# Kernel optimization log

Hardware: AMD Instinct MI355X
Metric: run time of the kernel (lower is better)

Reference implementation:

```python
import jax, jax.numpy as jnp
import numpy as np

EPS = 1e-5

def setup_inputs() -> dict:
    key = jax.random.key(0)
    ks = jax.random.split(key, 10)
    B, C, H, W, D = 1, 128, 20, 20, 20
    Cq = C // 8
    s = 0.05
    return {
        "x":   jax.random.normal(ks[0], (B, C, H, W, D), jnp.float32),
        "wq":  jax.random.normal(ks[1], (Cq, C), jnp.float32) * s,
        "bq":  jnp.zeros((Cq,), jnp.float32),
        "wk":  jax.random.normal(ks[2], (Cq, C), jnp.float32) * s,
        "bk":  jnp.zeros((Cq,), jnp.float32),
        "wv":  jax.random.normal(ks[3], (C, C), jnp.float32) * s,
        "bv":  jnp.zeros((C,), jnp.float32),
        "wa":  jax.random.normal(ks[4], (C, C), jnp.float32) * s,
        "ba":  jnp.zeros((C,), jnp.float32),
        "bn_w": jnp.ones((C,), jnp.float32),
        "bn_b": jnp.zeros((C,), jnp.float32),
    }

def reference(x, wq, bq, wk, bk, wv, bv, wa, ba, bn_w, bn_b):
    B, C, H, W, D = x.shape
    N = H * W * D
    xf = x.reshape(B, C, N)                                   # (B,C,N)
    # 1x1 conv projections = per-position channel matmuls
    q = jnp.einsum('oc,bcn->bno', wq, xf) + bq                # (B,N,Cq)
    k = jnp.einsum('oc,bcn->bon', wk, xf) + bk[:, None]       # (B,Cq,N)
    v = jnp.einsum('oc,bcn->bon', wv, xf) + bv[:, None]       # (B,C,N)
    # raw (unscaled) attention, softmax over key positions
    att = jax.nn.softmax(jnp.einsum('bnc,bcm->bnm', q, k), axis=-1)  # (B,N,N)
    # att_value[b,c,i] = sum_j value[b,c,j] * att[b,i,j]
    av = jnp.einsum('bcj,bij->bci', v, att)                   # (B,C,N)
    y = jnp.einsum('oc,bcn->bon', wa, av) + ba[:, None]       # (B,C,N)
    # BatchNorm (training mode): per-channel stats over batch + spatial
    mean = jnp.mean(y, axis=(0, 2), keepdims=True)
    var = jnp.var(y, axis=(0, 2), keepdims=True)
    y = (y - mean) * jax.lax.rsqrt(var + EPS) * bn_w[:, None] + bn_b[:, None]
    out = jax.nn.relu(y) + xf
    return out.reshape(B, C, H, W, D)
```

## Files before the change

### kernel.cpp

```cpp
#include <hip/hip_runtime.h>
#include <math.h>

#define N_POS 8000

typedef __bf16 bf16x8 __attribute__((ext_vector_type(8)));
typedef float  f32x4  __attribute__((ext_vector_type(4)));

#define MFMA(a,b,c) __builtin_amdgcn_mfma_f32_16x16x32_bf16((a),(b),(c),0,0,0)


#define GLOAD_LDS(gp, lp) \
    __builtin_amdgcn_global_load_lds( \
        (const __attribute__((address_space(1))) void*)(gp), \
        (__attribute__((address_space(3))) void*)(lp), 16, 0, 0)

__global__ __launch_bounds__(256) void qkv_kernel(
    const float* __restrict__ x,
    const float* __restrict__ wq, const float* __restrict__ bq,
    const float* __restrict__ wk, const float* __restrict__ bk,
    const float* __restrict__ wv, const float* __restrict__ bv,
    __bf16* __restrict__ q_bf, __bf16* __restrict__ k_bf, __bf16* __restrict__ v_bf)
{
    __shared__ __bf16 x_lds[32 * 136];
    __shared__ __bf16 v_out[128 * 36];

    const int t    = threadIdx.x;
    const int n0   = blockIdx.x * 32;
    const int lane = t & 63;
    const int w    = t >> 6;
    const int l15  = lane & 15;
    const int quad = lane >> 4;

    for (int r = 0; r < 4; ++r) {
        int f = r * 256 + t;
        int ch = f >> 3, n4 = f & 7;
        float4 xv = *reinterpret_cast<const float4*>(&x[ch * N_POS + n0 + n4 * 4]);
        x_lds[(n4 * 4 + 0) * 136 + ch] = (__bf16)xv.x;
        x_lds[(n4 * 4 + 1) * 136 + ch] = (__bf16)xv.y;
        x_lds[(n4 * 4 + 2) * 136 + ch] = (__bf16)xv.z;
        x_lds[(n4 * 4 + 3) * 136 + ch] = (__bf16)xv.w;
    }

    bf16x8 aw[3][4];
    f32x4  acc[3][2];
    const int nmt = (w < 2) ? 3 : 2;
    for (int mi = 0; mi < nmt; ++mi) {
        int mt = w + 4 * mi;
        const float *wrow, *brow;
        if (mt == 0)      { wrow = wq + l15 * 128;               brow = bq; }
        else if (mt == 1) { wrow = wk + l15 * 128;               brow = bk; }
        else              { wrow = wv + ((mt - 2) * 16 + l15) * 128;
                            brow = bv + (mt - 2) * 16; }
        for (int ks = 0; ks < 4; ++ks) {
            float4 f0 = *reinterpret_cast<const float4*>(wrow + ks * 32 + quad * 8);
            float4 f1 = *reinterpret_cast<const float4*>(wrow + ks * 32 + quad * 8 + 4);
            bf16x8 a;
            a[0]=(__bf16)f0.x; a[1]=(__bf16)f0.y; a[2]=(__bf16)f0.z; a[3]=(__bf16)f0.w;
            a[4]=(__bf16)f1.x; a[5]=(__bf16)f1.y; a[6]=(__bf16)f1.z; a[7]=(__bf16)f1.w;
            aw[mi][ks] = a;
        }
        for (int ni = 0; ni < 2; ++ni) {
            acc[mi][ni][0] = brow[quad * 4 + 0]; acc[mi][ni][1] = brow[quad * 4 + 1];
            acc[mi][ni][2] = brow[quad * 4 + 2]; acc[mi][ni][3] = brow[quad * 4 + 3];
        }
    }
    __syncthreads();

    for (int ks = 0; ks < 4; ++ks) {
        bf16x8 b0 = *reinterpret_cast<const bf16x8*>(&x_lds[(0  + l15) * 136 + ks * 32 + quad * 8]);
        bf16x8 b1 = *reinterpret_cast<const bf16x8*>(&x_lds[(16 + l15) * 136 + ks * 32 + quad * 8]);
        for (int mi = 0; mi < nmt; ++mi) {
            acc[mi][0] = MFMA(aw[mi][ks], b0, acc[mi][0]);
            acc[mi][1] = MFMA(aw[mi][ks], b1, acc[mi][1]);
        }
    }

    union S4 { short4 s; __bf16 b[4]; };
    for (int mi = 0; mi < nmt; ++mi) {
        int mt = w + 4 * mi;
        for (int ni = 0; ni < 2; ++ni) {
            S4 u;
            u.b[0]=(__bf16)acc[mi][ni][0]; u.b[1]=(__bf16)acc[mi][ni][1];
            u.b[2]=(__bf16)acc[mi][ni][2]; u.b[3]=(__bf16)acc[mi][ni][3];
            int n = n0 + ni * 16 + l15;
            if (mt == 0) {
                *reinterpret_cast<short4*>(&q_bf[n * 16 + quad * 4]) = u.s;
            } else if (mt == 1) {
                *reinterpret_cast<short4*>(&k_bf[n * 16 + quad * 4]) = u.s;
            } else {
                int ch0 = (mt - 2) * 16 + quad * 4;
                int nl  = ni * 16 + l15;
                v_out[(ch0 + 0) * 36 + nl] = u.b[0];
                v_out[(ch0 + 1) * 36 + nl] = u.b[1];
                v_out[(ch0 + 2) * 36 + nl] = u.b[2];
                v_out[(ch0 + 3) * 36 + nl] = u.b[3];
            }
        }
    }
    __syncthreads();
    for (int r = 0; r < 4; ++r) {
        int f = r * 256 + t;
        int ch = f >> 3, n4 = f & 7;
        int2 d = *reinterpret_cast<const int2*>(&v_out[ch * 36 + n4 * 4]);
        *reinterpret_cast<int2*>(&v_bf[ch * N_POS + n0 + n4 * 4]) = d;
    }
}

__global__ __launch_bounds__(256, 4) void attn_kernel(
    const __bf16* __restrict__ q_bf, const __bf16* __restrict__ k_bf,
    const __bf16* __restrict__ v_bf, float* __restrict__ av_part,
    float* __restrict__ l_part, int nsplit)
{
    __shared__ __bf16 v_buf[2][8192];
    __shared__ __bf16 k_buf[2][1024];
    __shared__ __bf16 p_lds[2048];

    const int t    = threadIdx.x;
    const int qt   = blockIdx.x % 250;
    const int sp   = blockIdx.x / 250;
    const int n0q  = qt * 32;
    const int lane = t & 63;
    const int w    = t >> 6;
    const int l15  = lane & 15;
    const int quad = lane >> 4;

    const int chL   = lane >> 3;
    const int vpart = (lane & 7) ^ chL;
    const int kkey  = lane >> 1;
    const int khalf = lane & 1;

    bf16x8 aq[2];
    for (int ni = 0; ni < 2; ++ni) {
        for (int j = 0; j < 8; ++j) aq[ni][j] = (__bf16)0.0f;
        if (quad < 2)
            aq[ni] = *reinterpret_cast<const bf16x8*>(
                &q_bf[(n0q + ni * 16 + l15) * 16 + quad * 8]);
    }
    bf16x8 ones;
    for (int j = 0; j < 8; ++j) ones[j] = (__bf16)1.0f;

    f32x4 acc[2][2];
    for (int mi = 0; mi < 2; ++mi)
        for (int ni = 0; ni < 2; ++ni)
            for (int r = 0; r < 4; ++r) acc[mi][ni][r] = 0.f;
    f32x4 lacc[2];
    for (int ni = 0; ni < 2; ++ni)
        for (int r = 0; r < 4; ++r) lacc[ni][r] = 0.f;

    const int base = 125 / nsplit, rem = 125 - base * nsplit;
    const int kt0  = sp * base + (sp < rem ? sp : rem);
    const int cnt  = base + (sp < rem ? 1 : 0);

    auto stage = [&](int kt, int buf) {
        const int n0k = kt * 64;
        for (int r = 0; r < 4; ++r) {
            int R = w * 4 + r;
            GLOAD_LDS(v_bf + (8 * R + chL) * N_POS + n0k + vpart * 8,
                      &v_buf[buf][R * 512]);
        }
        for (int h = 0; h < 2; ++h) {
            GLOAD_LDS(k_bf + (size_t)(n0k + h * 32 + kkey) * 16 + khalf * 8,
                      &k_buf[buf][h * 512]);
        }
    };

    stage(kt0, 0);

    const int oS  = w * 2 + (quad >> 1);
    const int sub = (quad & 1) * 4;

    for (int it = 0; it < cnt; ++it) {
        const int kt  = kt0 + it;
        const int cur = it & 1;
        __syncthreads();

        bf16x8 ak;
        for (int j = 0; j < 8; ++j) ak[j] = (__bf16)0.0f;
        if (quad < 2)
            ak = *reinterpret_cast<const bf16x8*>(
                &k_buf[cur][(w * 16 + l15) * 16 + quad * 8]);
        f32x4 s0, s1;
        for (int r = 0; r < 4; ++r) { s0[r] = 0.f; s1[r] = 0.f; }
        s0 = MFMA(ak, aq[0], s0);
        s1 = MFMA(ak, aq[1], s1);
        union SH { short4 sh; __bf16 b[4]; };
        {
            SH u;
            u.b[0] = (__bf16)__expf(s0[0]); u.b[1] = (__bf16)__expf(s0[1]);
            u.b[2] = (__bf16)__expf(s0[2]); u.b[3] = (__bf16)__expf(s0[3]);
            *reinterpret_cast<short4*>(&p_lds[(oS * 32 + l15) * 8 + sub]) = u.sh;
            u.b[0] = (__bf16)__expf(s1[0]); u.b[1] = (__bf16)__expf(s1[1]);
            u.b[2] = (__bf16)__expf(s1[2]); u.b[3] = (__bf16)__expf(s1[3]);
            *reinterpret_cast<short4*>(&p_lds[(oS * 32 + 16 + l15) * 8 + sub]) = u.sh;
        }
        __syncthreads();

        if (it + 1 < cnt) stage(kt + 1, cur ^ 1);

        const int chl = l15 & 7;
        for (int ks = 0; ks < 2; ++ks) {
            int pz = ((ks * 4 + quad) ^ chl);
            bf16x8 a0 = *reinterpret_cast<const bf16x8*>(
                &v_buf[cur][(((2 * w)     * 2 + (l15 >> 3)) * 64 + chl * 8 + pz) * 8]);
            bf16x8 a1 = *reinterpret_cast<const bf16x8*>(
                &v_buf[cur][(((2 * w + 1) * 2 + (l15 >> 3)) * 64 + chl * 8 + pz) * 8]);
            bf16x8 p0 = *reinterpret_cast<const bf16x8*>(
                &p_lds[((ks * 4 + quad) * 32 + 0  + l15) * 8]);
            bf16x8 p1 = *reinterpret_cast<const bf16x8*>(
                &p_lds[((ks * 4 + quad) * 32 + 16 + l15) * 8]);
            acc[0][0] = MFMA(a0, p0, acc[0][0]);
            acc[0][1] = MFMA(a0, p1, acc[0][1]);
            acc[1][0] = MFMA(a1, p0, acc[1][0]);
            acc[1][1] = MFMA(a1, p1, acc[1][1]);
            if (w == 0) {
                lacc[0] = MFMA(ones, p0, lacc[0]);
                lacc[1] = MFMA(ones, p1, lacc[1]);
            }
        }
    }

    float* dst = av_part + (size_t)sp * 1024000;
    for (int mi = 0; mi < 2; ++mi)
        for (int ni = 0; ni < 2; ++ni) {
            int n  = n0q + ni * 16 + l15;
            int ch = (2 * w + mi) * 16 + quad * 4;
            *reinterpret_cast<f32x4*>(&dst[n * 128 + ch]) = acc[mi][ni];
        }
    if (w == 0 && quad == 0) {
        l_part[sp * N_POS + n0q + 0  + l15] = lacc[0][0];
        l_part[sp * N_POS + n0q + 16 + l15] = lacc[1][0];
    }
}

__global__ __launch_bounds__(256) void proj_out_kernel(
    const float* __restrict__ av_part, const float* __restrict__ l_part,
    const float* __restrict__ wa, const float* __restrict__ ba,
    float* __restrict__ y_ws, float* __restrict__ bn_sum, float* __restrict__ bn_sumsq,
    int nsplit)
{
    __shared__ __bf16 b_lds[4096];

    const int t    = threadIdx.x;
    const int n0   = blockIdx.x * 32;
    const int lane = t & 63;
    const int w    = t >> 6;
    const int l15  = lane & 15;
    const int quad = lane >> 4;

    for (int r = 0; r < 2; ++r) {
        int g = r * 256 + t;
        int n = g >> 4, oc = g & 15;
        float l = 0.f;
        for (int s = 0; s < nsplit; ++s) l += l_part[s * N_POS + n0 + n];
        float4 a0 = make_float4(0.f, 0.f, 0.f, 0.f);
        float4 a1 = make_float4(0.f, 0.f, 0.f, 0.f);
        for (int s = 0; s < nsplit; ++s) {
            const float* p = av_part + (size_t)s * 1024000 + (n0 + n) * 128 + oc * 8;
            float4 u = *reinterpret_cast<const float4*>(p);
            float4 v = *reinterpret_cast<const float4*>(p + 4);
            a0.x += u.x; a0.y += u.y; a0.z += u.z; a0.w += u.w;
            a1.x += v.x; a1.y += v.y; a1.z += v.z; a1.w += v.w;
        }
        float inv = 1.f / l;
        union { int4 iv; __bf16 b[8]; } u;
        u.b[0]=(__bf16)(a0.x*inv); u.b[1]=(__bf16)(a0.y*inv);
        u.b[2]=(__bf16)(a0.z*inv); u.b[3]=(__bf16)(a0.w*inv);
        u.b[4]=(__bf16)(a1.x*inv); u.b[5]=(__bf16)(a1.y*inv);
        u.b[6]=(__bf16)(a1.z*inv); u.b[7]=(__bf16)(a1.w*inv);
        int A = (n >> 4) * 16 + oc;
        int slot = (n & 15) ^ (oc & 7);
        *reinterpret_cast<int4*>(&b_lds[(A * 16 + slot) * 8]) = u.iv;
    }

    bf16x8 aw[2][4];
    f32x4  acc[2][2];
    for (int mi = 0; mi < 2; ++mi) {
        int mt = 2 * w + mi;
        const float* wrow = wa + (mt * 16 + l15) * 128;
        for (int ks = 0; ks < 4; ++ks) {
            float4 f0 = *reinterpret_cast<const float4*>(wrow + ks * 32 + quad * 8);
            float4 f1 = *reinterpret_cast<const float4*>(wrow + ks * 32 + quad * 8 + 4);
            bf16x8 a;
            a[0]=(__bf16)f0.x; a[1]=(__bf16)f0.y; a[2]=(__bf16)f0.z; a[3]=(__bf16)f0.w;
            a[4]=(__bf16)f1.x; a[5]=(__bf16)f1.y; a[6]=(__bf16)f1.z; a[7]=(__bf16)f1.w;
            aw[mi][ks] = a;
        }
        for (int ni = 0; ni < 2; ++ni) {
            acc[mi][ni][0] = ba[mt * 16 + quad * 4 + 0];
            acc[mi][ni][1] = ba[mt * 16 + quad * 4 + 1];
            acc[mi][ni][2] = ba[mt * 16 + quad * 4 + 2];
            acc[mi][ni][3] = ba[mt * 16 + quad * 4 + 3];
        }
    }
    __syncthreads();

    for (int ks = 0; ks < 4; ++ks) {
        int oc = ks * 4 + quad;
        int slot = l15 ^ (oc & 7);
        bf16x8 b0 = *reinterpret_cast<const bf16x8*>(&b_lds[((0  + oc) * 16 + slot) * 8]);
        bf16x8 b1 = *reinterpret_cast<const bf16x8*>(&b_lds[((16 + oc) * 16 + slot) * 8]);
        for (int mi = 0; mi < 2; ++mi) {
            acc[mi][0] = MFMA(aw[mi][ks], b0, acc[mi][0]);
            acc[mi][1] = MFMA(aw[mi][ks], b1, acc[mi][1]);
        }
    }

    for (int mi = 0; mi < 2; ++mi) {
        for (int r = 0; r < 4; ++r) {
            int ch = (2 * w + mi) * 16 + quad * 4 + r;
            float v0 = acc[mi][0][r];
            float v1 = acc[mi][1][r];
            y_ws[ch * N_POS + n0 + 0  + l15] = v0;
            y_ws[ch * N_POS + n0 + 16 + l15] = v1;
            float s1 = v0 + v1;
            float s2 = v0 * v0 + v1 * v1;
#pragma unroll
            for (int off = 8; off >= 1; off >>= 1) {
                s1 += __shfl_xor(s1, off, 64);
                s2 += __shfl_xor(s2, off, 64);
            }
            if (l15 == 0) {
                atomicAdd(&bn_sum[ch],   s1);
                atomicAdd(&bn_sumsq[ch], s2);
            }
        }
    }
}

__global__ __launch_bounds__(256) void bn_relu_kernel(
    const float* __restrict__ y_ws, const float* __restrict__ x,
    const float* __restrict__ bn_sum, const float* __restrict__ bn_sumsq,
    const float* __restrict__ bn_w, const float* __restrict__ bn_b,
    float* __restrict__ out)
{
    const int i4 = blockIdx.x * 256 + threadIdx.x;
    const int c  = i4 / 2000;
    const float mean  = bn_sum[c]   * (1.f / 8000.f);
    const float var   = bn_sumsq[c] * (1.f / 8000.f) - mean * mean;
    const float rstd  = rsqrtf(var + 1e-5f);
    const float scale = bn_w[c] * rstd;
    const float shift = bn_b[c] - mean * scale;

    float4 y4 = reinterpret_cast<const float4*>(y_ws)[i4];
    float4 x4 = reinterpret_cast<const float4*>(x)[i4];
    float4 o4;
    o4.x = fmaxf(y4.x * scale + shift, 0.f) + x4.x;
    o4.y = fmaxf(y4.y * scale + shift, 0.f) + x4.y;
    o4.z = fmaxf(y4.z * scale + shift, 0.f) + x4.z;
    o4.w = fmaxf(y4.w * scale + shift, 0.f) + x4.w;
    reinterpret_cast<float4*>(out)[i4] = o4;
}

extern "C" void kernel_launch(void* const* d_in, const int* in_sizes, int n_in,
                              void* d_out, int out_size, void* d_ws, size_t ws_size,
                              hipStream_t stream)
{
    const float* x    = (const float*)d_in[0];
    const float* wq   = (const float*)d_in[1];
    const float* bq   = (const float*)d_in[2];
    const float* wk   = (const float*)d_in[3];
    const float* bk   = (const float*)d_in[4];
    const float* wv   = (const float*)d_in[5];
    const float* bv   = (const float*)d_in[6];
    const float* wa   = (const float*)d_in[7];
    const float* ba   = (const float*)d_in[8];
    const float* bn_w = (const float*)d_in[9];
    const float* bn_b = (const float*)d_in[10];
    float* out = (float*)d_out;

    const int nsplit = (ws_size >= 47937024ull) ? 10 : 5;

    char* base = (char*)d_ws;
    size_t avB = (size_t)nsplit * 4096000;
    float*  av_part = (float*)base;
    __bf16* q_bf    = (__bf16*)(base + avB);
    __bf16* k_bf    = (__bf16*)(base + avB + 256000);
    __bf16* v_bf    = (__bf16*)(base + avB + 512000);
    float*  l_part  = (float*)(base + avB + 2560000);
    float*  bn_sum   = (float*)(base + avB + 2560000 + (size_t)nsplit * 32000);
    float*  bn_sumsq = bn_sum + 128;
    float*  y_ws    = (float*)(base + avB + 2560000 + (size_t)nsplit * 32000 + 1024);

    hipMemsetAsync(bn_sum, 0, 1024, stream);
    qkv_kernel<<<250, 256, 0, stream>>>(x, wq, bq, wk, bk, wv, bv, q_bf, k_bf, v_bf);
    attn_kernel<<<250 * nsplit, 256, 0, stream>>>(q_bf, k_bf, v_bf,
                                                  av_part, l_part, nsplit);
    proj_out_kernel<<<250, 256, 0, stream>>>(av_part, l_part, wa, ba,
                                             y_ws, bn_sum, bn_sumsq, nsplit);
    bn_relu_kernel<<<1000, 256, 0, stream>>>(y_ws, x, bn_sum, bn_sumsq,
                                             bn_w, bn_b, out);
}
```

Baseline: 178.3 us.

## Store split attention partials in bf16 and double grid of qkv and projection kernels

Attention split-K partial outputs are now written as bf16 instead of fp32, halving the partial-buffer traffic between the attention and output-projection kernels. The qkv and output-projection kernels launch twice as many blocks, each doing half the channel tiles or 16 positions, to raise occupancy. The BN stats memset is folded into the qkv kernel, and the split count is fixed at 10 regardless of workspace size. Rounding partials to bf16 before the reduction adds some precision loss, and the fixed layout assumes the workspace is large enough.

```diff
diff --git a/kernel.cpp b/kernel.cpp
--- a/kernel.cpp
+++ b/kernel.cpp
@@ -2,6 +2,7 @@
 #include <math.h>
 
 #define N_POS 8000
+#define NSPLIT 10
 
 typedef __bf16 bf16x8 __attribute__((ext_vector_type(8)));
 typedef float  f32x4  __attribute__((ext_vector_type(4)));
@@ -19,17 +20,22 @@
     const float* __restrict__ wq, const float* __restrict__ bq,
     const float* __restrict__ wk, const float* __restrict__ bk,
     const float* __restrict__ wv, const float* __restrict__ bv,
-    __bf16* __restrict__ q_bf, __bf16* __restrict__ k_bf, __bf16* __restrict__ v_bf)
+    __bf16* __restrict__ q_bf, __bf16* __restrict__ k_bf, __bf16* __restrict__ v_bf,
+    float* __restrict__ bn_stats)
 {
     __shared__ __bf16 x_lds[32 * 136];
-    __shared__ __bf16 v_out[128 * 36];
+    __shared__ __bf16 v_out[80 * 36];
 
     const int t    = threadIdx.x;
-    const int n0   = blockIdx.x * 32;
+    const int nt   = blockIdx.x >> 1;
+    const int h    = blockIdx.x & 1;
+    const int n0   = nt * 32;
     const int lane = t & 63;
     const int w    = t >> 6;
     const int l15  = lane & 15;
     const int quad = lane >> 4;
+
+    if (blockIdx.x == 0) bn_stats[t] = 0.f;
 
     for (int r = 0; r < 4; ++r) {
         int f = r * 256 + t;
@@ -41,11 +47,13 @@
         x_lds[(n4 * 4 + 3) * 136 + ch] = (__bf16)xv.w;
     }
 
-    bf16x8 aw[3][4];
-    f32x4  acc[3][2];
-    const int nmt = (w < 2) ? 3 : 2;
+    const int nmt = (w == 0) ? 2 : 1;
+    int mts[2] = { h * 5 + w, h * 5 + 4 };
+
+    bf16x8 aw[2][4];
+    f32x4  acc[2][2];
     for (int mi = 0; mi < nmt; ++mi) {
-        int mt = w + 4 * mi;
+        int mt = mts[mi];
         const float *wrow, *brow;
         if (mt == 0)      { wrow = wq + l15 * 128;               brow = bq; }
         else if (mt == 1) { wrow = wk + l15 * 128;               brow = bk; }
@@ -77,7 +85,7 @@
 
     union S4 { short4 s; __bf16 b[4]; };
     for (int mi = 0; mi < nmt; ++mi) {
-        int mt = w + 4 * mi;
+        int mt = mts[mi];
         for (int ni = 0; ni < 2; ++ni) {
             S4 u;
             u.b[0]=(__bf16)acc[mi][ni][0]; u.b[1]=(__bf16)acc[mi][ni][1];
@@ -88,27 +96,27 @@
             } else if (mt == 1) {
                 *reinterpret_cast<short4*>(&k_bf[n * 16 + quad * 4]) = u.s;
             } else {
-                int ch0 = (mt - 2) * 16 + quad * 4;
-                int nl  = ni * 16 + l15;
-                v_out[(ch0 + 0) * 36 + nl] = u.b[0];
-                v_out[(ch0 + 1) * 36 + nl] = u.b[1];
-                v_out[(ch0 + 2) * 36 + nl] = u.b[2];
-                v_out[(ch0 + 3) * 36 + nl] = u.b[3];
+                int lv = (mt - 2) * 16 - h * 48 + quad * 4;
+                int nl = ni * 16 + l15;
+                v_out[(lv + 0) * 36 + nl] = u.b[0];
+                v_out[(lv + 1) * 36 + nl] = u.b[1];
+                v_out[(lv + 2) * 36 + nl] = u.b[2];
+                v_out[(lv + 3) * 36 + nl] = u.b[3];
             }
         }
     }
     __syncthreads();
-    for (int r = 0; r < 4; ++r) {
-        int f = r * 256 + t;
-        int ch = f >> 3, n4 = f & 7;
-        int2 d = *reinterpret_cast<const int2*>(&v_out[ch * 36 + n4 * 4]);
-        *reinterpret_cast<int2*>(&v_bf[ch * N_POS + n0 + n4 * 4]) = d;
+    const int nch = h ? 80 : 48;
+    for (int f = t; f < nch * 8; f += 256) {
+        int lc = f >> 3, n4 = f & 7;
+        int2 d = *reinterpret_cast<const int2*>(&v_out[lc * 36 + n4 * 4]);
+        *reinterpret_cast<int2*>(&v_bf[(lc + h * 48) * N_POS + n0 + n4 * 4]) = d;
     }
 }
 
 __global__ __launch_bounds__(256, 4) void attn_kernel(
     const __bf16* __restrict__ q_bf, const __bf16* __restrict__ k_bf,
-    const __bf16* __restrict__ v_bf, float* __restrict__ av_part,
+    const __bf16* __restrict__ v_bf, __bf16* __restrict__ av_part,
     float* __restrict__ l_part, int nsplit)
 {
     __shared__ __bf16 v_buf[2][8192];
@@ -219,12 +227,15 @@
         }
     }
 
-    float* dst = av_part + (size_t)sp * 1024000;
+    __bf16* dst = av_part + (size_t)sp * 1024000;
+    union SO { short4 sh; __bf16 b[4]; };
     for (int mi = 0; mi < 2; ++mi)
         for (int ni = 0; ni < 2; ++ni) {
-            int n  = n0q + ni * 16 + l15;
-            int ch = (2 * w + mi) * 16 + quad * 4;
-            *reinterpret_cast<f32x4*>(&dst[n * 128 + ch]) = acc[mi][ni];
+            SO o;
+            o.b[0] = (__bf16)acc[mi][ni][0]; o.b[1] = (__bf16)acc[mi][ni][1];
+            o.b[2] = (__bf16)acc[mi][ni][2]; o.b[3] = (__bf16)acc[mi][ni][3];
+            *reinterpret_cast<short4*>(
+                &dst[(size_t)(n0q + ni * 16 + l15) * 128 + (2 * w + mi) * 16 + quad * 4]) = o.sh;
         }
     if (w == 0 && quad == 0) {
         l_part[sp * N_POS + n0q + 0  + l15] = lacc[0][0];
@@ -233,47 +244,42 @@
 }
 
 __global__ __launch_bounds__(256) void proj_out_kernel(
-    const float* __restrict__ av_part, const float* __restrict__ l_part,
+    const __bf16* __restrict__ av_part, const float* __restrict__ l_part,
     const float* __restrict__ wa, const float* __restrict__ ba,
     float* __restrict__ y_ws, float* __restrict__ bn_sum, float* __restrict__ bn_sumsq,
     int nsplit)
 {
-    __shared__ __bf16 b_lds[4096];
+    __shared__ __bf16 b_lds[4352];
 
     const int t    = threadIdx.x;
-    const int n0   = blockIdx.x * 32;
+    const int n0   = blockIdx.x * 16;
     const int lane = t & 63;
     const int w    = t >> 6;
     const int l15  = lane & 15;
     const int quad = lane >> 4;
 
-    for (int r = 0; r < 2; ++r) {
-        int g = r * 256 + t;
-        int n = g >> 4, oc = g & 15;
+    {
+        int n = t >> 4, oc = t & 15;
         float l = 0.f;
         for (int s = 0; s < nsplit; ++s) l += l_part[s * N_POS + n0 + n];
-        float4 a0 = make_float4(0.f, 0.f, 0.f, 0.f);
-        float4 a1 = make_float4(0.f, 0.f, 0.f, 0.f);
+        float sum[8];
+#pragma unroll
+        for (int i = 0; i < 8; ++i) sum[i] = 0.f;
         for (int s = 0; s < nsplit; ++s) {
-            const float* p = av_part + (size_t)s * 1024000 + (n0 + n) * 128 + oc * 8;
-            float4 u = *reinterpret_cast<const float4*>(p);
-            float4 v = *reinterpret_cast<const float4*>(p + 4);
-            a0.x += u.x; a0.y += u.y; a0.z += u.z; a0.w += u.w;
-            a1.x += v.x; a1.y += v.y; a1.z += v.z; a1.w += v.w;
+            bf16x8 p = *reinterpret_cast<const bf16x8*>(
+                &av_part[(size_t)s * 1024000 + (size_t)(n0 + n) * 128 + oc * 8]);
+#pragma unroll
+            for (int i = 0; i < 8; ++i) sum[i] += (float)p[i];
         }
         float inv = 1.f / l;
         union { int4 iv; __bf16 b[8]; } u;
-        u.b[0]=(__bf16)(a0.x*inv); u.b[1]=(__bf16)(a0.y*inv);
-        u.b[2]=(__bf16)(a0.z*inv); u.b[3]=(__bf16)(a0.w*inv);
-        u.b[4]=(__bf16)(a1.x*inv); u.b[5]=(__bf16)(a1.y*inv);
-        u.b[6]=(__bf16)(a1.z*inv); u.b[7]=(__bf16)(a1.w*inv);
-        int A = (n >> 4) * 16 + oc;
-        int slot = (n & 15) ^ (oc & 7);
-        *reinterpret_cast<int4*>(&b_lds[(A * 16 + slot) * 8]) = u.iv;
+#pragma unroll
+        for (int i = 0; i < 8; ++i) u.b[i] = (__bf16)(sum[i] * inv);
+        *reinterpret_cast<int4*>(&b_lds[(oc * 17 + n) * 8]) = u.iv;
     }
 
     bf16x8 aw[2][4];
-    f32x4  acc[2][2];
+    f32x4  acc[2];
     for (int mi = 0; mi < 2; ++mi) {
         int mt = 2 * w + mi;
         const float* wrow = wa + (mt * 16 + l15) * 128;
@@ -285,35 +291,27 @@
             a[4]=(__bf16)f1.x; a[5]=(__bf16)f1.y; a[6]=(__bf16)f1.z; a[7]=(__bf16)f1.w;
             aw[mi][ks] = a;
         }
-        for (int ni = 0; ni < 2; ++ni) {
-            acc[mi][ni][0] = ba[mt * 16 + quad * 4 + 0];
-            acc[mi][ni][1] = ba[mt * 16 + quad * 4 + 1];
-            acc[mi][ni][2] = ba[mt * 16 + quad * 4 + 2];
-            acc[mi][ni][3] = ba[mt * 16 + quad * 4 + 3];
-        }
+        acc[mi][0] = ba[mt * 16 + quad * 4 + 0];
+        acc[mi][1] = ba[mt * 16 + quad * 4 + 1];
+        acc[mi][2] = ba[mt * 16 + quad * 4 + 2];
+        acc[mi][3] = ba[mt * 16 + quad * 4 + 3];
     }
     __syncthreads();
 
     for (int ks = 0; ks < 4; ++ks) {
-        int oc = ks * 4 + quad;
-        int slot = l15 ^ (oc & 7);
-        bf16x8 b0 = *reinterpret_cast<const bf16x8*>(&b_lds[((0  + oc) * 16 + slot) * 8]);
-        bf16x8 b1 = *reinterpret_cast<const bf16x8*>(&b_lds[((16 + oc) * 16 + slot) * 8]);
-        for (int mi = 0; mi < 2; ++mi) {
-            acc[mi][0] = MFMA(aw[mi][ks], b0, acc[mi][0]);
-            acc[mi][1] = MFMA(aw[mi][ks], b1, acc[mi][1]);
-        }
+        bf16x8 b = *reinterpret_cast<const bf16x8*>(
+            &b_lds[((ks * 4 + quad) * 17 + l15) * 8]);
+        acc[0] = MFMA(aw[0][ks], b, acc[0]);
+        acc[1] = MFMA(aw[1][ks], b, acc[1]);
     }
 
     for (int mi = 0; mi < 2; ++mi) {
+#pragma unroll
         for (int r = 0; r < 4; ++r) {
             int ch = (2 * w + mi) * 16 + quad * 4 + r;
-            float v0 = acc[mi][0][r];
-            float v1 = acc[mi][1][r];
-            y_ws[ch * N_POS + n0 + 0  + l15] = v0;
-            y_ws[ch * N_POS + n0 + 16 + l15] = v1;
-            float s1 = v0 + v1;
-            float s2 = v0 * v0 + v1 * v1;
+            float v = acc[mi][r];
+            y_ws[ch * N_POS + n0 + l15] = v;
+            float s1 = v, s2 = v * v;
 #pragma unroll
             for (int off = 8; off >= 1; off >>= 1) {
                 s1 += __shfl_xor(s1, off, 64);
@@ -368,25 +366,22 @@
     const float* bn_b = (const float*)d_in[10];
     float* out = (float*)d_out;
 
-    const int nsplit = (ws_size >= 47937024ull) ? 10 : 5;
-
     char* base = (char*)d_ws;
-    size_t avB = (size_t)nsplit * 4096000;
-    float*  av_part = (float*)base;
-    __bf16* q_bf    = (__bf16*)(base + avB);
-    __bf16* k_bf    = (__bf16*)(base + avB + 256000);
-    __bf16* v_bf    = (__bf16*)(base + avB + 512000);
-    float*  l_part  = (float*)(base + avB + 2560000);
-    float*  bn_sum   = (float*)(base + avB + 2560000 + (size_t)nsplit * 32000);
+    __bf16* av_part = (__bf16*)base;
+    __bf16* q_bf    = (__bf16*)(base + 20480000);
+    __bf16* k_bf    = (__bf16*)(base + 20736000);
+    __bf16* v_bf    = (__bf16*)(base + 20992000);
+    float*  l_part  = (float*)(base + 23040000);
+    float*  bn_sum   = (float*)(base + 23360000);
     float*  bn_sumsq = bn_sum + 128;
-    float*  y_ws    = (float*)(base + avB + 2560000 + (size_t)nsplit * 32000 + 1024);
-
-    hipMemsetAsync(bn_sum, 0, 1024, stream);
-    qkv_kernel<<<250, 256, 0, stream>>>(x, wq, bq, wk, bk, wv, bv, q_bf, k_bf, v_bf);
-    attn_kernel<<<250 * nsplit, 256, 0, stream>>>(q_bf, k_bf, v_bf,
-                                                  av_part, l_part, nsplit);
-    proj_out_kernel<<<250, 256, 0, stream>>>(av_part, l_part, wa, ba,
-                                             y_ws, bn_sum, bn_sumsq, nsplit);
+    float*  y_ws    = (float*)(base + 23361024);
+
+    qkv_kernel<<<500, 256, 0, stream>>>(x, wq, bq, wk, bk, wv, bv,
+                                        q_bf, k_bf, v_bf, bn_sum);
+    attn_kernel<<<250 * NSPLIT, 256, 0, stream>>>(q_bf, k_bf, v_bf,
+                                                  av_part, l_part, NSPLIT);
+    proj_out_kernel<<<500, 256, 0, stream>>>(av_part, l_part, wa, ba,
+                                             y_ws, bn_sum, bn_sumsq, NSPLIT);
     bn_relu_kernel<<<1000, 256, 0, stream>>>(y_ws, x, bn_sum, bn_sumsq,
                                              bn_w, bn_b, out);
 }
```

After: 258.4 us. +44.9%, slower.
